# Performance work log

Hardware: AMD Instinct MI355X
Metric: run time of the kernel (lower is better)

## Reference

```python
import jax, jax.numpy as jnp
import numpy as np

N_NODES = 50000
N_EDGES = 800000
D_IN = 16


def gcn_conv(x, edge_index, W, b, n_nodes):
    """PyG GCNConv: x' = D^{-1/2} (A + I) D^{-1/2} X W + b (add_self_loops=True)."""
    h = x @ W  # [N, d_out] - transform before propagate (small d => cheaper)
    src = jnp.concatenate([edge_index[0], jnp.arange(n_nodes)])  # add self-loops
    dst = jnp.concatenate([edge_index[1], jnp.arange(n_nodes)])
    deg = jax.ops.segment_sum(jnp.ones_like(dst, dtype=h.dtype), dst,
                              num_segments=n_nodes)  # in-degree incl. self-loop
    deg_inv_sqrt = jnp.where(deg > 0, jax.lax.rsqrt(deg), 0.0)
    norm = deg_inv_sqrt[src] * deg_inv_sqrt[dst]  # [E+N]
    msg = h[src] * norm[:, None]                  # gather + scale
    out = jax.ops.segment_sum(msg, dst, num_segments=n_nodes)  # scatter-add
    return out + b


def setup_inputs() -> dict:
    key = jax.random.key(0)
    ks = jax.random.split(key, 16)
    d = D_IN
    x = jax.random.normal(ks[0], (N_NODES, d), dtype=jnp.float32)
    edge_index = jax.random.randint(ks[1], (2, N_EDGES), 0, N_NODES, dtype=jnp.int64)

    def glorot(k, fan_in, fan_out):
        s = (6.0 / (fan_in + fan_out)) ** 0.5
        return jax.random.uniform(k, (fan_in, fan_out), jnp.float32, -s, s)

    return {
        "x": x,
        "edge_index": edge_index,
        "W1": glorot(ks[2], d, 2 * d),      "b1": jnp.zeros((2 * d,), jnp.float32),
        "W2": glorot(ks[3], 2 * d, 4 * d),  "b2": jnp.zeros((4 * d,), jnp.float32),
        "W3": glorot(ks[4], 4 * d, 8 * d),  "b3": jnp.zeros((8 * d,), jnp.float32),
        "Wl1": glorot(ks[5], 8 * d, 4 * d), "bl1": jnp.zeros((4 * d,), jnp.float32),
        "Wl2": glorot(ks[6], 4 * d, 2 * d), "bl2": jnp.zeros((2 * d,), jnp.float32),
        "Wl3": glorot(ks[7], 2 * d, d),     "bl3": jnp.zeros((d,), jnp.float32),
    }


def reference(x, edge_index, W1, b1, W2, b2, W3, b3, Wl1, bl1, Wl2, bl2, Wl3, bl3):
    n = x.shape[0]
    # note: original applies relu twice per conv; relu is idempotent
    out = jax.nn.relu(gcn_conv(x, edge_index, W1, b1, n))
    out = jax.nn.relu(gcn_conv(out, edge_index, W2, b2, n))
    out = jax.nn.relu(gcn_conv(out, edge_index, W3, b3, n))
    out = jax.nn.relu(out @ Wl1 + bl1)
    out = jax.nn.relu(out @ Wl2 + bl2)
    out = jax.nn.relu(out @ Wl3 + bl3)
    return out
```

## Files before the change

kernel.cpp:

```cpp
#include <hip/hip_runtime.h>

#define TPB 256
#define TE  2048
#define MAXB 6144

typedef _Float16 half_t;
typedef _Float16 half4 __attribute__((ext_vector_type(4)));
typedef _Float16 half8 __attribute__((ext_vector_type(8)));
typedef float float8v __attribute__((ext_vector_type(8)));

static inline int cdiv(int a, int b) { return (a + b - 1) / b; }


__global__ void k_zero_int(int* p, int n) {
    int i = blockIdx.x * blockDim.x + threadIdx.x;
    if (i < n) p[i] = 0;
}

__global__ void k_bhist(const int* __restrict__ dst, int* __restrict__ gcnt,
                        int e, int nb) {
    __shared__ int lc[256];
    for (int t = threadIdx.x; t < nb; t += TPB) lc[t] = 0;
    __syncthreads();
    for (int i = blockIdx.x * TPB + threadIdx.x; i < e; i += gridDim.x * TPB)
        atomicAdd(&lc[dst[i] >> 8], 1);
    __syncthreads();
    for (int t = threadIdx.x; t < nb; t += TPB) {
        int v = lc[t];
        if (v) atomicAdd(&gcnt[t], v);
    }
}

__global__ void __launch_bounds__(TPB)
k_binscatter(const int* __restrict__ src, const int* __restrict__ dst,
             const int* __restrict__ gcnt, int* __restrict__ bcur2,
             unsigned int* __restrict__ gbuf, int e, int nb) {
    __shared__ int lcnt[256], loffs[256], lcur[256], gres[256];
    __shared__ int ss[256];
    __shared__ unsigned int ldata[TE];
    const int tid = threadIdx.x;
    const int base = blockIdx.x * TE;
    const int cnt = min(TE, e - base);

    {
        int v = (tid < nb) ? gcnt[tid] : 0;
        ss[tid] = v;
        __syncthreads();
        for (int d = 1; d < 256; d <<= 1) {
            int x2 = (tid >= d) ? ss[tid - d] : 0;
            __syncthreads();
            ss[tid] += x2;
            __syncthreads();
        }
        gres[tid] = ss[tid] - v;
        lcnt[tid] = 0;
    }
    __syncthreads();

    unsigned int myv[TE / TPB];
    int myb[TE / TPB];
#pragma unroll
    for (int k = 0; k < TE / TPB; ++k) {
        int j = tid + k * TPB;
        if (j < cnt) {
            int d = dst[base + j], s = src[base + j];
            int b = d >> 8;
            myv[k] = ((unsigned)b << 24) | ((unsigned)(d & 255) << 16) | (unsigned)s;
            myb[k] = b;
            atomicAdd(&lcnt[b], 1);
        } else myb[k] = -1;
    }
    __syncthreads();
    {
        int v = (tid < nb) ? lcnt[tid] : 0;
        ss[tid] = v;
        __syncthreads();
        for (int d = 1; d < 256; d <<= 1) {
            int x2 = (tid >= d) ? ss[tid - d] : 0;
            __syncthreads();
            ss[tid] += x2;
            __syncthreads();
        }
        if (tid < nb) { loffs[tid] = ss[tid] - v; lcur[tid] = ss[tid] - v; }
    }
    __syncthreads();
    if (tid < nb && lcnt[tid]) gres[tid] += atomicAdd(&bcur2[tid], lcnt[tid]);
#pragma unroll
    for (int k = 0; k < TE / TPB; ++k) {
        if (myb[k] >= 0) {
            int p = atomicAdd(&lcur[myb[k]], 1);
            ldata[p] = myv[k];
        }
    }
    __syncthreads();
    for (int j = tid; j < cnt; j += TPB) {
        unsigned int v = ldata[j];
        int b = v >> 24;
        gbuf[gres[b] + (j - loffs[b])] = v & 0xFFFFFFu;
    }
}

__global__ void __launch_bounds__(TPB)
k_csr(const unsigned int* __restrict__ gbuf, const int* __restrict__ gcnt,
      const float* __restrict__ x, int* __restrict__ offs,
      float* __restrict__ dinv, unsigned short* __restrict__ ssrc,
      half_t* __restrict__ G, int n, int e, int nb) {
    __shared__ int ss[256], cnt[256], loffs2[256], lcur2[256];
    __shared__ float sdinv[256];
    __shared__ unsigned short stage[MAXB];
    const int b = blockIdx.x;
    const int t = threadIdx.x;

    {
        int v = (t < nb) ? gcnt[t] : 0;
        ss[t] = v;
        __syncthreads();
        for (int d = 1; d < 256; d <<= 1) {
            int x2 = (t >= d) ? ss[t - d] : 0;
            __syncthreads();
            ss[t] += x2;
            __syncthreads();
        }
    }
    const int s0 = (b > 0) ? ss[b - 1] : 0;
    const int s1 = ss[b];
    const int m = s1 - s0;
    __syncthreads();
    cnt[t] = 0;
    __syncthreads();
    for (int j = t; j < m; j += TPB)
        atomicAdd(&cnt[(gbuf[s0 + j] >> 16) & 255], 1);
    __syncthreads();
    {
        int v = cnt[t];
        ss[t] = v;
        __syncthreads();
        for (int d = 1; d < 256; d <<= 1) {
            int x2 = (t >= d) ? ss[t - d] : 0;
            __syncthreads();
            ss[t] += x2;
            __syncthreads();
        }
        loffs2[t] = ss[t] - v;
        lcur2[t] = ss[t] - v;
        float di = rsqrtf((float)v + 1.0f);
        sdinv[t] = di;
        int node = b * 256 + t;
        if (node < n) {
            offs[node] = s0 + loffs2[t];
            dinv[node] = di;
        }
    }
    __syncthreads();
    for (int j = t; j < m; j += TPB) {
        unsigned int v = gbuf[s0 + j];
        int p = atomicAdd(&lcur2[(v >> 16) & 255], 1);
        stage[p] = (unsigned short)(v & 0xFFFFu);
    }
    __syncthreads();
    for (int j = t; j < m; j += TPB) ssrc[s0 + j] = stage[j];
    if (b == 0 && t == 0) offs[n] = e;

    const int base = b * 256;
    const int cn = min(256, n - base);
    const float4* X4 = (const float4*)x;
    half4* G4 = (half4*)G;
    for (int j = t; j < cn * 4; j += TPB) {
        int nl = j >> 2, k4 = j & 3;
        float4 v = X4[(size_t)(base + nl) * 4 + k4];
        float d = sdinv[nl];
        half4 h;
        h.x = (half_t)(v.x * d); h.y = (half_t)(v.y * d);
        h.z = (half_t)(v.z * d); h.w = (half_t)(v.w * d);
        G4[(size_t)(base + nl) * 4 + k4] = h;
    }
}

template<int DI, int DO, int R, bool SCALE, bool OUT_HALF, bool WHALF>
__global__ void __launch_bounds__(TPB, 4)
k_conv(const int* __restrict__ offs, const unsigned short* __restrict__ ssrc,
       const half_t* __restrict__ G, const float* __restrict__ dinv,
       const float* __restrict__ W, const float* __restrict__ b,
       void* __restrict__ outp, int n) {
    constexpr int CT = DO / 4;
    constexpr int RT = TPB / CT;
    constexpr int TM = RT * R;
    constexpr int K4 = DI / 4;
    constexpr int PX = K4 + 1;
    constexpr int C  = DI / 8;
    static_assert(TM * C == TPB, "gather/gemm tile mismatch");
    __shared__ float4 sW4[WHALF ? 1 : DI * CT];
    __shared__ half4  sWh[WHALF ? DI * CT : 1];
    __shared__ float4 sX4[TM * PX];
    __shared__ int soffs[TM + 1];
    const int tid = threadIdx.x;
    const int r0 = blockIdx.x * TM;

    const float4* Wg = (const float4*)W;
    for (int t = tid; t < DI * CT; t += TPB) {
        float4 w = Wg[t];
        if (WHALF) {
            half4 h;
            h.x = (half_t)w.x; h.y = (half_t)w.y;
            h.z = (half_t)w.z; h.w = (half_t)w.w;
            sWh[t] = h;
        } else {
            sW4[t] = w;
        }
    }
    if (tid <= TM) soffs[tid] = offs[min(r0 + tid, n)];
    __syncthreads();

    {
        int lrow = tid / C;
        int gc = tid - lrow * C;
        int row = r0 + lrow;
        float8v acc;
#pragma unroll
        for (int q = 0; q < 8; ++q) acc[q] = 0.f;
        if (row < n) {
            const half8* Grow = (const half8*)G;
            half8 hs = Grow[(size_t)row * C + gc];
#pragma unroll
            for (int q = 0; q < 8; ++q) acc[q] = (float)hs[q];
            int s0 = soffs[lrow], s1 = soffs[lrow + 1];
            int j = s0;
            for (; j + 7 < s1; j += 8) {
                half8 g0 = Grow[(size_t)ssrc[j + 0] * C + gc];
                half8 g1 = Grow[(size_t)ssrc[j + 1] * C + gc];
                half8 g2 = Grow[(size_t)ssrc[j + 2] * C + gc];
                half8 g3 = Grow[(size_t)ssrc[j + 3] * C + gc];
                half8 g4 = Grow[(size_t)ssrc[j + 4] * C + gc];
                half8 g5 = Grow[(size_t)ssrc[j + 5] * C + gc];
                half8 g6 = Grow[(size_t)ssrc[j + 6] * C + gc];
                half8 g7 = Grow[(size_t)ssrc[j + 7] * C + gc];
#pragma unroll
                for (int q = 0; q < 8; ++q)
                    acc[q] += (((float)g0[q] + (float)g1[q]) + ((float)g2[q] + (float)g3[q]))
                            + (((float)g4[q] + (float)g5[q]) + ((float)g6[q] + (float)g7[q]));
            }
            for (; j + 3 < s1; j += 4) {
                half8 g0 = Grow[(size_t)ssrc[j + 0] * C + gc];
                half8 g1 = Grow[(size_t)ssrc[j + 1] * C + gc];
                half8 g2 = Grow[(size_t)ssrc[j + 2] * C + gc];
                half8 g3 = Grow[(size_t)ssrc[j + 3] * C + gc];
#pragma unroll
                for (int q = 0; q < 8; ++q)
                    acc[q] += ((float)g0[q] + (float)g1[q]) + ((float)g2[q] + (float)g3[q]);
            }
            for (; j < s1; ++j) {
                half8 ga = Grow[(size_t)ssrc[j] * C + gc];
#pragma unroll
                for (int q = 0; q < 8; ++q) acc[q] += (float)ga[q];
            }
            float di = dinv[row];
#pragma unroll
            for (int q = 0; q < 8; ++q) acc[q] *= di;
        }
        sX4[lrow * PX + 2 * gc]     = make_float4(acc[0], acc[1], acc[2], acc[3]);
        sX4[lrow * PX + 2 * gc + 1] = make_float4(acc[4], acc[5], acc[6], acc[7]);
    }
    __syncthreads();

    const int c = tid & (CT - 1);
    const int rg = tid / CT;
    const int rbase = rg * R;
    float4 acc[R];
#pragma unroll
    for (int r = 0; r < R; ++r) acc[r] = make_float4(0.f, 0.f, 0.f, 0.f);

#pragma unroll 2
    for (int k4 = 0; k4 < K4; ++k4) {
        float4 xv[R];
#pragma unroll
        for (int r = 0; r < R; ++r) xv[r] = sX4[(rbase + r) * PX + k4];
#pragma unroll
        for (int kk = 0; kk < 4; ++kk) {
            float4 wv;
            if (WHALF) {
                half4 wh = sWh[(k4 * 4 + kk) * CT + c];
                wv = make_float4((float)wh.x, (float)wh.y, (float)wh.z, (float)wh.w);
            } else {
                wv = sW4[(k4 * 4 + kk) * CT + c];
            }
#pragma unroll
            for (int r = 0; r < R; ++r) {
                float xs = (kk == 0) ? xv[r].x : (kk == 1) ? xv[r].y
                         : (kk == 2) ? xv[r].z : xv[r].w;
                acc[r].x += xs * wv.x; acc[r].y += xs * wv.y;
                acc[r].z += xs * wv.z; acc[r].w += xs * wv.w;
            }
        }
    }

    float4 bc = ((const float4*)b)[c];
#pragma unroll
    for (int r = 0; r < R; ++r) {
        int row = r0 + rbase + r;
        if (row < n) {
            float4 o;
            o.x = fmaxf(acc[r].x + bc.x, 0.f);
            o.y = fmaxf(acc[r].y + bc.y, 0.f);
            o.z = fmaxf(acc[r].z + bc.z, 0.f);
            o.w = fmaxf(acc[r].w + bc.w, 0.f);
            if (SCALE) {
                float d = dinv[row];
                o.x *= d; o.y *= d; o.z *= d; o.w *= d;
            }
            if (OUT_HALF) {
                half4 h;
                h.x = (half_t)o.x; h.y = (half_t)o.y;
                h.z = (half_t)o.z; h.w = (half_t)o.w;
                ((half4*)outp)[(size_t)row * CT + c] = h;
            } else {
                ((float4*)outp)[(size_t)row * CT + c] = o;
            }
        }
    }
}

__global__ void __launch_bounds__(256, 2)
k_head(const half_t* __restrict__ X,
       const float* __restrict__ W1, const float* __restrict__ b1,
       const float* __restrict__ W2, const float* __restrict__ b2,
       const float* __restrict__ W3, const float* __restrict__ b3,
       float* __restrict__ out, int n) {
    __shared__ half_t hW1[128 * 64];
    __shared__ half_t hW2[64 * 32];
    __shared__ half_t hW3[32 * 16];
    __shared__ float h1[64 * 65];
    __shared__ float h2[64 * 33];
    const int tid = threadIdx.x;
    const int r0 = blockIdx.x * 64;

    for (int t = tid; t < 128 * 64; t += 256) hW1[t] = (half_t)W1[t];
    for (int t = tid; t < 64 * 32; t += 256) hW2[t] = (half_t)W2[t];
    for (int t = tid; t < 32 * 16; t += 256) hW3[t] = (half_t)W3[t];
    __syncthreads();

    {
        const int c4 = tid & 15;
        const int rowg = tid >> 4;
        const half8* Xr = (const half8*)X;
        float acc[4][4];
#pragma unroll
        for (int r = 0; r < 4; ++r)
#pragma unroll
            for (int j = 0; j < 4; ++j) acc[r][j] = 0.f;
        for (int k8 = 0; k8 < 16; ++k8) {
            half8 xh[4];
#pragma unroll
            for (int r = 0; r < 4; ++r) {
                int row = r0 + rowg * 4 + r;
                if (row < n) xh[r] = Xr[(size_t)row * 16 + k8];
                else { half8 z; for (int q = 0; q < 8; ++q) z[q] = (half_t)0.f; xh[r] = z; }
            }
#pragma unroll
            for (int q = 0; q < 8; ++q) {
                int k = k8 * 8 + q;
                half4 w = *(const half4*)&hW1[k * 64 + c4 * 4];
                float w0 = (float)w.x, w1 = (float)w.y, w2 = (float)w.z, w3 = (float)w.w;
#pragma unroll
                for (int r = 0; r < 4; ++r) {
                    float xs = (float)xh[r][q];
                    acc[r][0] += xs * w0; acc[r][1] += xs * w1;
                    acc[r][2] += xs * w2; acc[r][3] += xs * w3;
                }
            }
        }
        float4 bc = ((const float4*)b1)[c4];
#pragma unroll
        for (int r = 0; r < 4; ++r) {
            int rl = rowg * 4 + r;
            h1[rl * 65 + c4 * 4 + 0] = fmaxf(acc[r][0] + bc.x, 0.f);
            h1[rl * 65 + c4 * 4 + 1] = fmaxf(acc[r][1] + bc.y, 0.f);
            h1[rl * 65 + c4 * 4 + 2] = fmaxf(acc[r][2] + bc.z, 0.f);
            h1[rl * 65 + c4 * 4 + 3] = fmaxf(acc[r][3] + bc.w, 0.f);
        }
    }
    __syncthreads();

    {
        const int c4 = tid & 7;
        const int rowg = tid >> 3;
        float acc[2][4];
#pragma unroll
        for (int r = 0; r < 2; ++r)
#pragma unroll
            for (int j = 0; j < 4; ++j) acc[r][j] = 0.f;
#pragma unroll 4
        for (int k = 0; k < 64; ++k) {
            half4 w = *(const half4*)&hW2[k * 32 + c4 * 4];
            float w0 = (float)w.x, w1 = (float)w.y, w2 = (float)w.z, w3 = (float)w.w;
#pragma unroll
            for (int r = 0; r < 2; ++r) {
                float xs = h1[(rowg * 2 + r) * 65 + k];
                acc[r][0] += xs * w0; acc[r][1] += xs * w1;
                acc[r][2] += xs * w2; acc[r][3] += xs * w3;
            }
        }
        float4 bc = ((const float4*)b2)[c4];
#pragma unroll
        for (int r = 0; r < 2; ++r) {
            int rl = rowg * 2 + r;
            h2[rl * 33 + c4 * 4 + 0] = fmaxf(acc[r][0] + bc.x, 0.f);
            h2[rl * 33 + c4 * 4 + 1] = fmaxf(acc[r][1] + bc.y, 0.f);
            h2[rl * 33 + c4 * 4 + 2] = fmaxf(acc[r][2] + bc.z, 0.f);
            h2[rl * 33 + c4 * 4 + 3] = fmaxf(acc[r][3] + bc.w, 0.f);
        }
    }
    __syncthreads();

    {
        const int c4 = tid & 3;
        const int rl = tid >> 2;
        float a0 = 0.f, a1 = 0.f, a2 = 0.f, a3 = 0.f;
#pragma unroll 4
        for (int k = 0; k < 32; ++k) {
            half4 w = *(const half4*)&hW3[k * 16 + c4 * 4];
            float xs = h2[rl * 33 + k];
            a0 += xs * (float)w.x; a1 += xs * (float)w.y;
            a2 += xs * (float)w.z; a3 += xs * (float)w.w;
        }
        int row = r0 + rl;
        if (row < n) {
            float4 bc = ((const float4*)b3)[c4];
            float4 o;
            o.x = fmaxf(a0 + bc.x, 0.f);
            o.y = fmaxf(a1 + bc.y, 0.f);
            o.z = fmaxf(a2 + bc.z, 0.f);
            o.w = fmaxf(a3 + bc.w, 0.f);
            ((float4*)out)[(size_t)row * 4 + c4] = o;
        }
    }
}

extern "C" void kernel_launch(void* const* d_in, const int* in_sizes, int n_in,
                              void* d_out, int out_size, void* d_ws, size_t ws_size,
                              hipStream_t stream) {
    const float* x   = (const float*)d_in[0];
    const int*   ei  = (const int*)d_in[1];
    const float* W1  = (const float*)d_in[2];
    const float* bb1 = (const float*)d_in[3];
    const float* W2  = (const float*)d_in[4];
    const float* bb2 = (const float*)d_in[5];
    const float* W3  = (const float*)d_in[6];
    const float* bb3 = (const float*)d_in[7];
    const float* Wl1 = (const float*)d_in[8];
    const float* bl1 = (const float*)d_in[9];
    const float* Wl2 = (const float*)d_in[10];
    const float* bl2 = (const float*)d_in[11];
    const float* Wl3 = (const float*)d_in[12];
    const float* bl3 = (const float*)d_in[13];
    float* out = (float*)d_out;

    const int n = in_sizes[0] / 16;
    const int e = in_sizes[1] / 2;
    const int* src = ei;
    const int* dst = ei + e;
    const int nb = cdiv(n, 256);

    char* p = (char*)d_ws;
    auto alloc = [&](size_t bytes) {
        char* r = p;
        p += (bytes + 255) & ~(size_t)255;
        return r;
    };
    float*          dinv   = (float*)         alloc((size_t)n * 4);
    int*            offs   = (int*)           alloc((size_t)(n + 1) * 4);
    int*            gcnt   = (int*)           alloc(256 * 4);
    int*            bcur2  = (int*)           alloc(256 * 4);
    unsigned int*   gbuf   = (unsigned int*)  alloc((size_t)e * 4);
    unsigned short* ssrc   = (unsigned short*)alloc((size_t)e * 2);
    half_t*         H1     = (half_t*)        alloc((size_t)n * 64 * 2);
    half_t*         H2     = (half_t*)        alloc((size_t)n * 32 * 2);
    half_t*         X3h    = (half_t*)        alloc((size_t)n * 128 * 2);

    k_zero_int<<<2, 256, 0, stream>>>(gcnt, 512);
    k_bhist<<<512, TPB, 0, stream>>>(dst, gcnt, e, nb);
    k_binscatter<<<cdiv(e, TE), TPB, 0, stream>>>(src, dst, gcnt, bcur2, gbuf, e, nb);
    k_csr<<<nb, TPB, 0, stream>>>(gbuf, gcnt, x, offs, dinv, ssrc, H1, n, e, nb);

    k_conv<16, 32, 4, true, true, false><<<cdiv(n, 128), TPB, 0, stream>>>(
        offs, ssrc, H1, dinv, W1, bb1, H2, n);
    k_conv<32, 64, 4, true, true, false><<<cdiv(n, 64), TPB, 0, stream>>>(
        offs, ssrc, H2, dinv, W2, bb2, H1, n);
    k_conv<64, 128, 4, false, true, true><<<cdiv(n, 32), TPB, 0, stream>>>(
        offs, ssrc, H1, dinv, W3, bb3, X3h, n);

    k_head<<<cdiv(n, 64), 256, 0, stream>>>(X3h, Wl1, bl1, Wl2, bl2, Wl3, bl3, out, n);
}
```

Baseline: 214.6 us.

## Drop histogram pass via fixed-capacity buckets and pad CSR rows to 8-edge chunks

Removes the global destination histogram kernel by giving each 256-node bucket a fixed MAXB-slot region in the staging buffer, so binscatter appends with per-bucket atomics and no prefix scan. The CSR build pads each node's neighbour list to a multiple of 8, filling the padding with a sentinel node n whose feature row is zeroed. The conv gather then reads 8 packed indices per uint4 load with no remainder loops. The cost is extra padded gathers of the zero row and a hard limit of MAXB edges per bucket, which would overflow on skewed degree distributions.

```diff
diff --git a/kernel.cpp b/kernel.cpp
--- a/kernel.cpp
+++ b/kernel.cpp
@@ -17,44 +17,17 @@
     if (i < n) p[i] = 0;
 }
 
-__global__ void k_bhist(const int* __restrict__ dst, int* __restrict__ gcnt,
-                        int e, int nb) {
-    __shared__ int lc[256];
-    for (int t = threadIdx.x; t < nb; t += TPB) lc[t] = 0;
-    __syncthreads();
-    for (int i = blockIdx.x * TPB + threadIdx.x; i < e; i += gridDim.x * TPB)
-        atomicAdd(&lc[dst[i] >> 8], 1);
-    __syncthreads();
-    for (int t = threadIdx.x; t < nb; t += TPB) {
-        int v = lc[t];
-        if (v) atomicAdd(&gcnt[t], v);
-    }
-}
-
 __global__ void __launch_bounds__(TPB)
 k_binscatter(const int* __restrict__ src, const int* __restrict__ dst,
-             const int* __restrict__ gcnt, int* __restrict__ bcur2,
-             unsigned int* __restrict__ gbuf, int e, int nb) {
+             int* __restrict__ bcur, unsigned int* __restrict__ gbuf,
+             int e, int nb) {
     __shared__ int lcnt[256], loffs[256], lcur[256], gres[256];
     __shared__ int ss[256];
     __shared__ unsigned int ldata[TE];
     const int tid = threadIdx.x;
     const int base = blockIdx.x * TE;
     const int cnt = min(TE, e - base);
-
-    {
-        int v = (tid < nb) ? gcnt[tid] : 0;
-        ss[tid] = v;
-        __syncthreads();
-        for (int d = 1; d < 256; d <<= 1) {
-            int x2 = (tid >= d) ? ss[tid - d] : 0;
-            __syncthreads();
-            ss[tid] += x2;
-            __syncthreads();
-        }
-        gres[tid] = ss[tid] - v;
-        lcnt[tid] = 0;
-    }
+    lcnt[tid] = 0;
     __syncthreads();
 
     unsigned int myv[TE / TPB];
@@ -72,7 +45,7 @@
     }
     __syncthreads();
     {
-        int v = (tid < nb) ? lcnt[tid] : 0;
+        int v = lcnt[tid];
         ss[tid] = v;
         __syncthreads();
         for (int d = 1; d < 256; d <<= 1) {
@@ -81,10 +54,12 @@
             ss[tid] += x2;
             __syncthreads();
         }
-        if (tid < nb) { loffs[tid] = ss[tid] - v; lcur[tid] = ss[tid] - v; }
-    }
-    __syncthreads();
-    if (tid < nb && lcnt[tid]) gres[tid] += atomicAdd(&bcur2[tid], lcnt[tid]);
+        loffs[tid] = ss[tid] - v;
+        lcur[tid] = ss[tid] - v;
+    }
+    __syncthreads();
+    if (tid < nb && lcnt[tid])
+        gres[tid] = tid * MAXB + atomicAdd(&bcur[tid], lcnt[tid]);
 #pragma unroll
     for (int k = 0; k < TE / TPB; ++k) {
         if (myb[k] >= 0) {
@@ -101,19 +76,28 @@
 }
 
 __global__ void __launch_bounds__(TPB)
-k_csr(const unsigned int* __restrict__ gbuf, const int* __restrict__ gcnt,
+k_csr(const unsigned int* __restrict__ gbuf, const int* __restrict__ bcur,
       const float* __restrict__ x, int* __restrict__ offs,
-      float* __restrict__ dinv, unsigned short* __restrict__ ssrc,
-      half_t* __restrict__ G, int n, int e, int nb) {
-    __shared__ int ss[256], cnt[256], loffs2[256], lcur2[256];
+      unsigned short* __restrict__ nch, float* __restrict__ dinv,
+      unsigned short* __restrict__ ssrc, half_t* __restrict__ G, int n, int nb) {
+    __shared__ int ss[256], cnt[256], loffs2[256], lcur2[256], pcnt[256];
     __shared__ float sdinv[256];
     __shared__ unsigned short stage[MAXB];
     const int b = blockIdx.x;
     const int t = threadIdx.x;
-
-    {
-        int v = (t < nb) ? gcnt[t] : 0;
-        ss[t] = v;
+    const int s0 = b * MAXB;
+    const int m = bcur[b];
+
+    cnt[t] = 0;
+    __syncthreads();
+    for (int j = t; j < m; j += TPB)
+        atomicAdd(&cnt[(gbuf[s0 + j] >> 16) & 255], 1);
+    __syncthreads();
+    {
+        int v = cnt[t];
+        int pv = (v + 7) & ~7;
+        pcnt[t] = pv;
+        ss[t] = pv;
         __syncthreads();
         for (int d = 1; d < 256; d <<= 1) {
             int x2 = (t >= d) ? ss[t - d] : 0;
@@ -121,33 +105,14 @@
             ss[t] += x2;
             __syncthreads();
         }
-    }
-    const int s0 = (b > 0) ? ss[b - 1] : 0;
-    const int s1 = ss[b];
-    const int m = s1 - s0;
-    __syncthreads();
-    cnt[t] = 0;
-    __syncthreads();
-    for (int j = t; j < m; j += TPB)
-        atomicAdd(&cnt[(gbuf[s0 + j] >> 16) & 255], 1);
-    __syncthreads();
-    {
-        int v = cnt[t];
-        ss[t] = v;
-        __syncthreads();
-        for (int d = 1; d < 256; d <<= 1) {
-            int x2 = (t >= d) ? ss[t - d] : 0;
-            __syncthreads();
-            ss[t] += x2;
-            __syncthreads();
-        }
-        loffs2[t] = ss[t] - v;
-        lcur2[t] = ss[t] - v;
+        loffs2[t] = ss[t] - pv;
+        lcur2[t] = ss[t] - pv;
         float di = rsqrtf((float)v + 1.0f);
         sdinv[t] = di;
         int node = b * 256 + t;
         if (node < n) {
             offs[node] = s0 + loffs2[t];
+            nch[node] = (unsigned short)(pv >> 3);
             dinv[node] = di;
         }
     }
@@ -158,8 +123,13 @@
         stage[p] = (unsigned short)(v & 0xFFFFu);
     }
     __syncthreads();
-    for (int j = t; j < m; j += TPB) ssrc[s0 + j] = stage[j];
-    if (b == 0 && t == 0) offs[n] = e;
+    {
+        int base2 = loffs2[t] + cnt[t], end2 = loffs2[t] + pcnt[t];
+        for (int q = base2; q < end2; ++q) stage[q] = (unsigned short)n;
+    }
+    __syncthreads();
+    const int tot = ss[255];
+    for (int j = t; j < tot; j += TPB) ssrc[s0 + j] = stage[j];
 
     const int base = b * 256;
     const int cn = min(256, n - base);
@@ -174,11 +144,13 @@
         h.z = (half_t)(v.z * d); h.w = (half_t)(v.w * d);
         G4[(size_t)(base + nl) * 4 + k4] = h;
     }
-}
-
-template<int DI, int DO, int R, bool SCALE, bool OUT_HALF, bool WHALF>
+    if (b == 0 && t < 4) G4[(size_t)n * 4 + t] = half4{0, 0, 0, 0};
+}
+
+template<int DI, int DO, int R, bool SCALE, bool OUT_HALF, bool WHALF, bool ZSENT>
 __global__ void __launch_bounds__(TPB, 4)
-k_conv(const int* __restrict__ offs, const unsigned short* __restrict__ ssrc,
+k_conv(const int* __restrict__ offs, const unsigned short* __restrict__ nch,
+       const unsigned short* __restrict__ ssrc,
        const half_t* __restrict__ G, const float* __restrict__ dinv,
        const float* __restrict__ W, const float* __restrict__ b,
        void* __restrict__ outp, int n) {
@@ -192,7 +164,8 @@
     __shared__ float4 sW4[WHALF ? 1 : DI * CT];
     __shared__ half4  sWh[WHALF ? DI * CT : 1];
     __shared__ float4 sX4[TM * PX];
-    __shared__ int soffs[TM + 1];
+    __shared__ int soffs[TM];
+    __shared__ unsigned short snch[TM];
     const int tid = threadIdx.x;
     const int r0 = blockIdx.x * TM;
 
@@ -208,7 +181,11 @@
             sW4[t] = w;
         }
     }
-    if (tid <= TM) soffs[tid] = offs[min(r0 + tid, n)];
+    if (tid < TM) {
+        int row = r0 + tid;
+        soffs[tid] = (row < n) ? offs[row] : 0;
+        snch[tid] = (row < n) ? nch[row] : (unsigned short)0;
+    }
     __syncthreads();
 
     {
@@ -223,35 +200,26 @@
             half8 hs = Grow[(size_t)row * C + gc];
 #pragma unroll
             for (int q = 0; q < 8; ++q) acc[q] = (float)hs[q];
-            int s0 = soffs[lrow], s1 = soffs[lrow + 1];
-            int j = s0;
-            for (; j + 7 < s1; j += 8) {
-                half8 g0 = Grow[(size_t)ssrc[j + 0] * C + gc];
-                half8 g1 = Grow[(size_t)ssrc[j + 1] * C + gc];
-                half8 g2 = Grow[(size_t)ssrc[j + 2] * C + gc];
-                half8 g3 = Grow[(size_t)ssrc[j + 3] * C + gc];
-                half8 g4 = Grow[(size_t)ssrc[j + 4] * C + gc];
-                half8 g5 = Grow[(size_t)ssrc[j + 5] * C + gc];
-                half8 g6 = Grow[(size_t)ssrc[j + 6] * C + gc];
-                half8 g7 = Grow[(size_t)ssrc[j + 7] * C + gc];
+            const int nchunks = snch[lrow];
+            const uint4* sv = (const uint4*)(ssrc + soffs[lrow]);
+            for (int k = 0; k < nchunks; ++k) {
+                uint4 pk = sv[k];
+                int a0 = pk.x & 0xFFFF, a1 = pk.x >> 16;
+                int a2 = pk.y & 0xFFFF, a3 = pk.y >> 16;
+                int a4 = pk.z & 0xFFFF, a5 = pk.z >> 16;
+                int a6 = pk.w & 0xFFFF, a7 = pk.w >> 16;
+                half8 g0 = Grow[(size_t)a0 * C + gc];
+                half8 g1 = Grow[(size_t)a1 * C + gc];
+                half8 g2 = Grow[(size_t)a2 * C + gc];
+                half8 g3 = Grow[(size_t)a3 * C + gc];
+                half8 g4 = Grow[(size_t)a4 * C + gc];
+                half8 g5 = Grow[(size_t)a5 * C + gc];
+                half8 g6 = Grow[(size_t)a6 * C + gc];
+                half8 g7 = Grow[(size_t)a7 * C + gc];
 #pragma unroll
                 for (int q = 0; q < 8; ++q)
                     acc[q] += (((float)g0[q] + (float)g1[q]) + ((float)g2[q] + (float)g3[q]))
                             + (((float)g4[q] + (float)g5[q]) + ((float)g6[q] + (float)g7[q]));
-            }
-            for (; j + 3 < s1; j += 4) {
-                half8 g0 = Grow[(size_t)ssrc[j + 0] * C + gc];
-                half8 g1 = Grow[(size_t)ssrc[j + 1] * C + gc];
-                half8 g2 = Grow[(size_t)ssrc[j + 2] * C + gc];
-                half8 g3 = Grow[(size_t)ssrc[j + 3] * C + gc];
-#pragma unroll
-                for (int q = 0; q < 8; ++q)
-                    acc[q] += ((float)g0[q] + (float)g1[q]) + ((float)g2[q] + (float)g3[q]);
-            }
-            for (; j < s1; ++j) {
-                half8 ga = Grow[(size_t)ssrc[j] * C + gc];
-#pragma unroll
-                for (int q = 0; q < 8; ++q) acc[q] += (float)ga[q];
             }
             float di = dinv[row];
 #pragma unroll
@@ -317,6 +285,8 @@
             }
         }
     }
+    if (ZSENT && OUT_HALF && blockIdx.x == 0 && tid < CT)
+        ((half4*)outp)[(size_t)n * CT + tid] = half4{0, 0, 0, 0};
 }
 
 __global__ void __launch_bounds__(256, 2)
@@ -466,27 +436,26 @@
         p += (bytes + 255) & ~(size_t)255;
         return r;
     };
-    float*          dinv   = (float*)         alloc((size_t)n * 4);
-    int*            offs   = (int*)           alloc((size_t)(n + 1) * 4);
-    int*            gcnt   = (int*)           alloc(256 * 4);
-    int*            bcur2  = (int*)           alloc(256 * 4);
-    unsigned int*   gbuf   = (unsigned int*)  alloc((size_t)e * 4);
-    unsigned short* ssrc   = (unsigned short*)alloc((size_t)e * 2);
-    half_t*         H1     = (half_t*)        alloc((size_t)n * 64 * 2);
-    half_t*         H2     = (half_t*)        alloc((size_t)n * 32 * 2);
-    half_t*         X3h    = (half_t*)        alloc((size_t)n * 128 * 2);
-
-    k_zero_int<<<2, 256, 0, stream>>>(gcnt, 512);
-    k_bhist<<<512, TPB, 0, stream>>>(dst, gcnt, e, nb);
-    k_binscatter<<<cdiv(e, TE), TPB, 0, stream>>>(src, dst, gcnt, bcur2, gbuf, e, nb);
-    k_csr<<<nb, TPB, 0, stream>>>(gbuf, gcnt, x, offs, dinv, ssrc, H1, n, e, nb);
-
-    k_conv<16, 32, 4, true, true, false><<<cdiv(n, 128), TPB, 0, stream>>>(
-        offs, ssrc, H1, dinv, W1, bb1, H2, n);
-    k_conv<32, 64, 4, true, true, false><<<cdiv(n, 64), TPB, 0, stream>>>(
-        offs, ssrc, H2, dinv, W2, bb2, H1, n);
-    k_conv<64, 128, 4, false, true, true><<<cdiv(n, 32), TPB, 0, stream>>>(
-        offs, ssrc, H1, dinv, W3, bb3, X3h, n);
+    float*          dinv = (float*)         alloc((size_t)n * 4);
+    int*            offs = (int*)           alloc((size_t)n * 4);
+    unsigned short* nch  = (unsigned short*)alloc((size_t)n * 2);
+    int*            bcur = (int*)           alloc(256 * 4);
+    unsigned int*   gbuf = (unsigned int*)  alloc((size_t)nb * MAXB * 4);
+    unsigned short* ssrc = (unsigned short*)alloc((size_t)nb * MAXB * 2);
+    half_t*         H1   = (half_t*)        alloc((size_t)(n + 1) * 64 * 2);
+    half_t*         H2   = (half_t*)        alloc((size_t)(n + 1) * 32 * 2);
+    half_t*         X3h  = (half_t*)        alloc((size_t)n * 128 * 2);
+
+    k_zero_int<<<1, 256, 0, stream>>>(bcur, 256);
+    k_binscatter<<<cdiv(e, TE), TPB, 0, stream>>>(src, dst, bcur, gbuf, e, nb);
+    k_csr<<<nb, TPB, 0, stream>>>(gbuf, bcur, x, offs, nch, dinv, ssrc, H1, n, nb);
+
+    k_conv<16, 32, 4, true, true, false, true><<<cdiv(n, 128), TPB, 0, stream>>>(
+        offs, nch, ssrc, H1, dinv, W1, bb1, H2, n);
+    k_conv<32, 64, 4, true, true, false, true><<<cdiv(n, 64), TPB, 0, stream>>>(
+        offs, nch, ssrc, H2, dinv, W2, bb2, H1, n);
+    k_conv<64, 128, 4, false, true, true, false><<<cdiv(n, 32), TPB, 0, stream>>>(
+        offs, nch, ssrc, H1, dinv, W3, bb3, X3h, n);
 
     k_head<<<cdiv(n, 64), 256, 0, stream>>>(X3h, Wl1, bl1, Wl2, bl2, Wl3, bl3, out, n);
 }
```

New measurement: 196.4 us. 1.09x faster.
